# Kernel optimization log

Hardware: AMD Instinct MI355X
Metric: run time of the kernel (lower is better)

## Reference

```python
import jax, jax.numpy as jnp
import numpy as np

WS = 6        # window size -> N = 36 tokens per window
HEADS = 16

def _rel_index(ws):
    coords = np.stack(np.meshgrid(np.arange(ws), np.arange(ws), indexing='ij')).reshape(2, -1)
    rel = coords[:, :, None] - coords[:, None, :] + (ws - 1)
    return jnp.asarray(rel[0] * (2 * ws - 1) + rel[1])  # (N, N) int

REL_IDX = _rel_index(WS)

def _ln(x, g, b, eps=1e-5):
    m = x.mean(-1, keepdims=True)
    v = x.var(-1, keepdims=True)
    return (x - m) / jnp.sqrt(v + eps) * g + b

def setup_inputs() -> dict:
    key = jax.random.key(0)
    ks = jax.random.split(key, 6)
    B, H, W, C = 16, 96, 96, 512
    hid = 4 * C
    s = 0.02
    return {
        'x': jax.random.normal(ks[0], (B, H, W, C), jnp.float32),
        'w_qkv': jax.random.normal(ks[1], (C, 3 * C), jnp.float32) * s,
        'w_proj': jax.random.normal(ks[2], (C, C), jnp.float32) * s,
        'b_proj': jnp.zeros((C,), jnp.float32),
        'rel_bias': jax.random.normal(ks[3], ((2 * WS - 1) ** 2, HEADS), jnp.float32) * s,
        'ln1_g': jnp.ones((C,), jnp.float32), 'ln1_b': jnp.zeros((C,), jnp.float32),
        'ln2_g': jnp.ones((C,), jnp.float32), 'ln2_b': jnp.zeros((C,), jnp.float32),
        'w_fc1': jax.random.normal(ks[4], (C, hid), jnp.float32) * s,
        'b_fc1': jnp.zeros((hid,), jnp.float32),
        'w_fc2': jax.random.normal(ks[5], (hid, C), jnp.float32) * s,
        'b_fc2': jnp.zeros((C,), jnp.float32),
    }

def reference(x, w_qkv, w_proj, b_proj, rel_bias, ln1_g, ln1_b, ln2_g, ln2_b, w_fc1, b_fc1, w_fc2, b_fc2):
    B, H, W, C = x.shape
    h, d, N = HEADS, C // HEADS, WS * WS
    nh, nw = H // WS, W // WS
    # window partition: (B,H,W,C) -> (B*nh*nw, N, C)
    xw = x.reshape(B, nh, WS, nw, WS, C).transpose(0, 1, 3, 2, 4, 5).reshape(B * nh * nw, N, C)
    xn = _ln(xw, ln1_g, ln1_b)
    qkv = xn @ w_qkv
    q, k, v = jnp.split(qkv, 3, axis=-1)
    to_heads = lambda t: t.reshape(-1, N, h, d).transpose(0, 2, 1, 3)  # (B_, h, N, d)
    q = to_heads(q) * (d ** -0.5)
    k = to_heads(k)
    v = to_heads(v)
    attn = jnp.einsum('bhnd,bhmd->bhnm', q, k)
    bias = rel_bias[REL_IDX.reshape(-1)].reshape(N, N, h).transpose(2, 0, 1)  # (h, N, N)
    attn = jax.nn.softmax(attn + bias[None], axis=-1)
    o = jnp.einsum('bhnm,bhmd->bhnd', attn, v).transpose(0, 2, 1, 3).reshape(-1, N, C)
    o = o @ w_proj + b_proj
    # un-window; NOTE: source has no residual around attention (x is replaced)
    x2 = o.reshape(B, nh, nw, WS, WS, C).transpose(0, 1, 3, 2, 4, 5).reshape(B, H, W, C)
    xm = _ln(x2, ln2_g, ln2_b)
    mlp = jax.nn.gelu(xm @ w_fc1 + b_fc1, approximate=False) @ w_fc2 + b_fc2
    return x2 + mlp
```

## Files before the change

### kernel.cpp

```cpp
#include <hip/hip_runtime.h>
#include <stdint.h>

#define TOK 147456
#define CCH 512

typedef __attribute__((ext_vector_type(8))) short short8;
typedef __attribute__((ext_vector_type(4))) float f32x4;

struct alignas(8) US4 { unsigned short a, b, c, d; };

typedef __attribute__((address_space(3))) void lds_void;
typedef const __attribute__((address_space(1))) void gbl_void;

__device__ inline void gload16(const void* g, void* l) {
    __builtin_amdgcn_global_load_lds((gbl_void*)g, (lds_void*)l, 16, 0, 0);
}

__device__ inline unsigned short f2bf(float f) {
    union { float f; unsigned u; } v{f};
    unsigned r = v.u + 0x7fffu + ((v.u >> 16) & 1u);
    return (unsigned short)(r >> 16);
}
__device__ inline float bf2f(unsigned short h) {
    union { unsigned u; float f; } v; v.u = ((unsigned)h) << 16; return v.f;
}

__global__ void wprep(const float* __restrict__ in, unsigned short* __restrict__ out,
                      int K, int N) {
    int idx = blockIdx.x * 256 + threadIdx.x;
    if (idx >= K * N) return;
    int k = idx / N, n = idx % N;
    out[(size_t)n * K + k] = f2bf(in[idx]);
}

__global__ void biasprep(const float* __restrict__ rb, float* __restrict__ bb) {
    int idx = blockIdx.x * 256 + threadIdx.x;
    if (idx >= 16 * 48 * 48) return;
    int h = idx / 2304, rem = idx % 2304, r = rem / 48, c = rem % 48;
    float v = -1e9f;
    if (r < 36 && c < 36) {
        int dy = r / 6 - c / 6 + 5;
        int dx = r % 6 - c % 6 + 5;
        v = rb[(dy * 11 + dx) * 16 + h];
    }
    bb[idx] = v;
}

__global__ __launch_bounds__(256) void ln_k(const float* __restrict__ x,
                                            const float* __restrict__ g,
                                            const float* __restrict__ b,
                                            unsigned short* __restrict__ out, int ntok) {
    int lane = threadIdx.x & 63;
    int tok = blockIdx.x * 4 + (threadIdx.x >> 6);
    if (tok >= ntok) return;
    const float4* xr = (const float4*)(x + (size_t)tok * CCH);
    float4 v0 = xr[lane], v1 = xr[lane + 64];
    float s  = v0.x + v0.y + v0.z + v0.w + v1.x + v1.y + v1.z + v1.w;
    float s2 = v0.x*v0.x + v0.y*v0.y + v0.z*v0.z + v0.w*v0.w
             + v1.x*v1.x + v1.y*v1.y + v1.z*v1.z + v1.w*v1.w;
#pragma unroll
    for (int off = 32; off; off >>= 1) { s += __shfl_xor(s, off); s2 += __shfl_xor(s2, off); }
    float mean = s * (1.f / 512.f);
    float var  = s2 * (1.f / 512.f) - mean * mean;
    float inv  = rsqrtf(var + 1e-5f);
    const float4* gp = (const float4*)g;
    const float4* bp = (const float4*)b;
    float4 g0 = gp[lane], g1 = gp[lane + 64], b0 = bp[lane], b1 = bp[lane + 64];
    US4 o0, o1;
    o0.a = f2bf((v0.x - mean) * inv * g0.x + b0.x);
    o0.b = f2bf((v0.y - mean) * inv * g0.y + b0.y);
    o0.c = f2bf((v0.z - mean) * inv * g0.z + b0.z);
    o0.d = f2bf((v0.w - mean) * inv * g0.w + b0.w);
    o1.a = f2bf((v1.x - mean) * inv * g1.x + b1.x);
    o1.b = f2bf((v1.y - mean) * inv * g1.y + b1.y);
    o1.c = f2bf((v1.z - mean) * inv * g1.z + b1.z);
    o1.d = f2bf((v1.w - mean) * inv * g1.w + b1.w);
    unsigned short* op = out + (size_t)tok * CCH;
    *(US4*)(op + 4 * lane)       = o0;
    *(US4*)(op + 256 + 4 * lane) = o1;
}

__global__ __launch_bounds__(256) void ln_bf(const unsigned short* __restrict__ x,
                                             const float* __restrict__ g,
                                             const float* __restrict__ b,
                                             unsigned short* __restrict__ out, int ntok) {
    int lane = threadIdx.x & 63;
    int tok = blockIdx.x * 4 + (threadIdx.x >> 6);
    if (tok >= ntok) return;
    short8 v = *(const short8*)(x + (size_t)tok * CCH + lane * 8);
    float f[8];
#pragma unroll
    for (int j = 0; j < 8; ++j) f[j] = bf2f((unsigned short)v[j]);
    float s = 0.f, s2 = 0.f;
#pragma unroll
    for (int j = 0; j < 8; ++j) { s += f[j]; s2 += f[j] * f[j]; }
#pragma unroll
    for (int off = 32; off; off >>= 1) { s += __shfl_xor(s, off); s2 += __shfl_xor(s2, off); }
    float mean = s * (1.f / 512.f);
    float var  = s2 * (1.f / 512.f) - mean * mean;
    float inv  = rsqrtf(var + 1e-5f);
    const float4* gp = (const float4*)g + lane * 2;
    const float4* bp = (const float4*)b + lane * 2;
    float4 g0 = gp[0], g1 = gp[1], b0 = bp[0], b1 = bp[1];
    float gg[8] = {g0.x, g0.y, g0.z, g0.w, g1.x, g1.y, g1.z, g1.w};
    float bb[8] = {b0.x, b0.y, b0.z, b0.w, b1.x, b1.y, b1.z, b1.w};
    short8 o;
#pragma unroll
    for (int j = 0; j < 8; ++j) o[j] = (short)f2bf((f[j] - mean) * inv * gg[j] + bb[j]);
    *(short8*)(out + (size_t)tok * CCH + lane * 8) = o;
}

__global__ __launch_bounds__(256) void attn_mfma(const unsigned short* __restrict__ qkv,
                                                 const float* __restrict__ biasb,
                                                 unsigned short* __restrict__ o) {
    __shared__ __align__(16) unsigned short p_lds[4][48 * 64];
    __shared__ __align__(16) unsigned short v_lds[4][32 * 64];

    int tid  = threadIdx.x;
    int wv   = tid >> 6;
    int lane = tid & 63;
    int l15  = lane & 15;
    int g    = lane >> 4;

    int wid = blockIdx.x * 4 + wv;
    int h   = wid & 15;
    int win = wid >> 4;
    int img  = win >> 8;
    int wrow = (win >> 4) & 15;
    int wcol = win & 15;
    int tok_base = (img * 96 + wrow * 6) * 96 + wcol * 6;

    unsigned short* pw = p_lds[wv];
    unsigned short* vw = v_lds[wv];

    #define TOKOF(r) (tok_base + (r) + 90 * ((r) / 6))

    short8 z8 = {};
    for (int e = lane; e < 224; e += 64) {
        if (e < 128) {
            int ch = e >> 2, kst = 32 + (e & 3) * 8;
            *(short8*)(vw + ch * 64 + (kst ^ ((ch & 7) << 3))) = z8;
        } else {
            int ee = e - 128; int q = ee >> 1, kst = 48 + (ee & 1) * 8;
            *(short8*)(pw + q * 64 + (kst ^ ((q & 7) << 3))) = z8;
        }
    }

    for (int e = lane; e < 144; e += 64) {
        int r = e >> 2, c0 = (e & 3) * 8;
        short8 vv = *(const short8*)(qkv + (size_t)TOKOF(r) * 1536 + 1024 + h * 32 + c0);
#pragma unroll
        for (int j = 0; j < 8; ++j) {
            int ch = c0 + j;
            vw[ch * 64 + (r ^ ((ch & 7) << 3))] = (unsigned short)vv[j];
        }
    }

    short8 qf[3], kf[3];
#pragma unroll
    for (int t = 0; t < 3; ++t) {
        int r = t * 16 + l15;
        if (r < 36) {
            size_t ba = (size_t)TOKOF(r) * 1536 + h * 32 + g * 8;
            qf[t] = *(const short8*)(qkv + ba);
            kf[t] = *(const short8*)(qkv + ba + 512);
        } else { qf[t] = z8; kf[t] = z8; }
    }

    f32x4 s[3][3] = {};
#pragma unroll
    for (int mt = 0; mt < 3; ++mt)
#pragma unroll
        for (int nt = 0; nt < 3; ++nt)
            s[mt][nt] = __builtin_amdgcn_mfma_f32_16x16x32_bf16(qf[mt], kf[nt], s[mt][nt], 0, 0, 0);

    const float SCALE = 0.17677669529663687f;
    const float* bh = biasb + h * 2304;
#pragma unroll
    for (int mt = 0; mt < 3; ++mt) {
#pragma unroll
        for (int r = 0; r < 4; ++r) {
            int row = mt * 16 + g * 4 + r;
            const float* bb = bh + row * 48 + l15;
            float v0 = fmaf(s[mt][0][r], SCALE, bb[0]);
            float v1 = fmaf(s[mt][1][r], SCALE, bb[16]);
            float v2 = fmaf(s[mt][2][r], SCALE, bb[32]);
            float m = fmaxf(fmaxf(v0, v1), v2);
#pragma unroll
            for (int off = 1; off < 16; off <<= 1) m = fmaxf(m, __shfl_xor(m, off));
            float e0 = __expf(v0 - m), e1 = __expf(v1 - m), e2 = __expf(v2 - m);
            float sm = e0 + e1 + e2;
#pragma unroll
            for (int off = 1; off < 16; off <<= 1) sm += __shfl_xor(sm, off);
            float inv = 1.f / sm;
            int sw = (row & 7) << 3;
            unsigned short* pr = pw + row * 64;
            pr[(l15)      ^ sw] = f2bf(e0 * inv);
            pr[(16 + l15) ^ sw] = f2bf(e1 * inv);
            pr[(32 + l15) ^ sw] = f2bf(e2 * inv);
        }
    }

    f32x4 oacc[3][2] = {};
#pragma unroll
    for (int ks = 0; ks < 2; ++ks) {
        int kst = ks * 32 + g * 8;
        short8 bfr[2];
#pragma unroll
        for (int nt = 0; nt < 2; ++nt) {
            int c = nt * 16 + l15;
            bfr[nt] = *(const short8*)(vw + c * 64 + (kst ^ ((c & 7) << 3)));
        }
#pragma unroll
        for (int mt = 0; mt < 3; ++mt) {
            int q = mt * 16 + l15;
            short8 pa = *(const short8*)(pw + q * 64 + (kst ^ ((q & 7) << 3)));
#pragma unroll
            for (int nt = 0; nt < 2; ++nt)
                oacc[mt][nt] = __builtin_amdgcn_mfma_f32_16x16x32_bf16(pa, bfr[nt], oacc[mt][nt], 0, 0, 0);
        }
    }

#pragma unroll
    for (int mt = 0; mt < 3; ++mt) {
#pragma unroll
        for (int r = 0; r < 4; ++r) {
            int q = mt * 16 + g * 4 + r;
            if (q < 36) {
                size_t rb = (size_t)TOKOF(q) * 512 + h * 32;
#pragma unroll
                for (int nt = 0; nt < 2; ++nt)
                    o[rb + nt * 16 + l15] = f2bf(oacc[mt][nt][r]);
            }
        }
    }
    #undef TOKOF
}

template <int EPI>
__global__ __launch_bounds__(512, 4) void gemm8(const unsigned short* __restrict__ A,
                                                const unsigned short* __restrict__ Bt,
                                                int M, int N, int K,
                                                const float* __restrict__ bias,
                                                const unsigned short* __restrict__ resid,
                                                void* __restrict__ Cout) {
    extern __shared__ char lds[];
    int tid = threadIdx.x;
    int w = tid >> 6, lane = tid & 63;
    int l15 = lane & 15, grp = lane >> 4;
    int wm = w >> 2, wn = w & 3;

    int nbn = N >> 8;
    int nwg = gridDim.x;
    int q = nwg >> 3, r = nwg & 7;
    int xcd = blockIdx.x & 7, pos_ = blockIdx.x >> 3;
    int wgid = (xcd < r ? xcd * (q + 1) : r * (q + 1) + (xcd - r) * q) + pos_;
    int bm = wgid / nbn, bn = wgid % nbn;

    int NT = K >> 5;

    int u = (tid & 7) ^ ((tid >> 3) & 7);
    int srow = ((tid >> 3) << 1) + (u >> 2);
    int scol = (u & 3) * 8;
    const unsigned short* aSrc = A  + ((size_t)bm * 128 + srow) * (size_t)K + scol;
    const unsigned short* bSrc = Bt + ((size_t)bn * 256 + srow) * (size_t)K + scol;

    #define STAGE(t) do { char* s_ = lds + ((t) % 3) * 24576; size_t ko_ = (size_t)(t) * 32; \
        gload16(aSrc + ko_,                   s_ + tid * 16); \
        gload16(bSrc + ko_,                   s_ + 8192  + tid * 16); \
        gload16(bSrc + ko_ + (size_t)128 * K, s_ + 16384 + tid * 16); } while (0)

    int rpos = (grp + (l15 & 1) * 4) ^ ((l15 >> 1) & 7);
    int aRd = (wm * 32 + (l15 >> 1)) * 128 + rpos * 16;
    int bRd = 8192 + (wn * 32 + (l15 >> 1)) * 128 + rpos * 16;

    f32x4 acc[4][4] = {};

    STAGE(0); STAGE(1);

    for (int t = 0; t < NT; ++t) {
        if (t + 2 < NT) {
            STAGE(t + 2);
            asm volatile("s_waitcnt vmcnt(6)" ::: "memory");
        } else if (t + 1 < NT) {
            asm volatile("s_waitcnt vmcnt(3)" ::: "memory");
        } else {
            asm volatile("s_waitcnt vmcnt(0)" ::: "memory");
        }
        __builtin_amdgcn_s_barrier();
        char* sb = lds + (t % 3) * 24576;
        short8 af[4], bf[4];
#pragma unroll
        for (int m = 0; m < 4; ++m) af[m] = *(const short8*)(sb + aRd + m * 1024);
#pragma unroll
        for (int n = 0; n < 4; ++n) bf[n] = *(const short8*)(sb + bRd + n * 1024);
        asm volatile("s_waitcnt lgkmcnt(0)" ::: "memory");
        __builtin_amdgcn_sched_barrier(0);
        __builtin_amdgcn_s_setprio(1);
#pragma unroll
        for (int m = 0; m < 4; ++m)
#pragma unroll
            for (int n = 0; n < 4; ++n)
                acc[m][n] = __builtin_amdgcn_mfma_f32_16x16x32_bf16(af[m], bf[n], acc[m][n], 0, 0, 0);
        __builtin_amdgcn_s_setprio(0);
        __builtin_amdgcn_s_barrier();
    }
    #undef STAGE

    int row0 = bm * 128 + wm * 64 + grp * 4;
    int col0 = bn * 256 + wn * 64 + l15;
#pragma unroll
    for (int m = 0; m < 4; ++m) {
#pragma unroll
        for (int n = 0; n < 4; ++n) {
            int col = col0 + n * 16;
            float bv = (EPI == 0) ? 0.f : bias[col];
#pragma unroll
            for (int r2 = 0; r2 < 4; ++r2) {
                int row = row0 + m * 16 + r2;
                size_t idx = (size_t)row * N + col;
                float val = acc[m][n][r2] + bv;
                if (EPI == 0) {
                    ((unsigned short*)Cout)[idx] = f2bf(val);
                } else if (EPI == 1) {
                    ((unsigned short*)Cout)[idx] = f2bf(val);
                } else if (EPI == 2) {
                    float u3 = val * val * val;
                    float z2 = 1.5957691216f * (val + 0.044715f * u3);
                    float e = __expf(z2);
                    float th = 1.f - 2.f / (e + 1.f);
                    float ge = 0.5f * val * (1.f + th);
                    ((unsigned short*)Cout)[idx] = f2bf(ge);
                } else {
                    ((float*)Cout)[idx] = val + bf2f(resid[idx]);
                }
            }
        }
    }
}

extern "C" void kernel_launch(void* const* d_in, const int* in_sizes, int n_in,
                              void* d_out, int out_size, void* d_ws, size_t ws_size,
                              hipStream_t stream) {
    const float* x       = (const float*)d_in[0];
    const float* w_qkv   = (const float*)d_in[1];
    const float* w_proj  = (const float*)d_in[2];
    const float* b_proj  = (const float*)d_in[3];
    const float* relb    = (const float*)d_in[4];
    const float* ln1g    = (const float*)d_in[5];
    const float* ln1b    = (const float*)d_in[6];
    const float* ln2g    = (const float*)d_in[7];
    const float* ln2b    = (const float*)d_in[8];
    const float* w_fc1   = (const float*)d_in[9];
    const float* b_fc1   = (const float*)d_in[10];
    const float* w_fc2   = (const float*)d_in[11];
    const float* b_fc2   = (const float*)d_in[12];
    float* out = (float*)d_out;

    hipFuncSetAttribute(reinterpret_cast<const void*>(&gemm8<0>),
                        hipFuncAttributeMaxDynamicSharedMemorySize, 73728);
    hipFuncSetAttribute(reinterpret_cast<const void*>(&gemm8<1>),
                        hipFuncAttributeMaxDynamicSharedMemorySize, 73728);
    hipFuncSetAttribute(reinterpret_cast<const void*>(&gemm8<2>),
                        hipFuncAttributeMaxDynamicSharedMemorySize, 73728);
    hipFuncSetAttribute(reinterpret_cast<const void*>(&gemm8<3>),
                        hipFuncAttributeMaxDynamicSharedMemorySize, 73728);

    char* w = (char*)d_ws;
    unsigned short* wT_qkv  = (unsigned short*)w; w += (size_t)1536 * 512 * 2;
    unsigned short* wT_proj = (unsigned short*)w; w += (size_t)512  * 512 * 2;
    unsigned short* wT_fc1  = (unsigned short*)w; w += (size_t)2048 * 512 * 2;
    unsigned short* wT_fc2  = (unsigned short*)w; w += (size_t)512  * 2048 * 2;
    float* biasb            = (float*)w;          w += (size_t)16 * 48 * 48 * 4;
    size_t wbytes = (size_t)(w - (char*)d_ws);

    int nchunk = 16;
    for (int c = 1; c <= 16; c *= 2) {
        size_t tokc = TOK / c;
        if (wbytes + tokc * 6144 <= ws_size) { nchunk = c; break; }
    }
    size_t tokc = TOK / nchunk;
    unsigned short* buf1 = (unsigned short*)w;
    unsigned short* buf2 = (unsigned short*)(w + tokc * 1024);
    unsigned short* buf3 = (unsigned short*)(w + tokc * 5120);

    wprep<<<(512 * 1536 + 255) / 256, 256, 0, stream>>>(w_qkv,  wT_qkv,  512, 1536);
    wprep<<<(512 * 512  + 255) / 256, 256, 0, stream>>>(w_proj, wT_proj, 512, 512);
    wprep<<<(512 * 2048 + 255) / 256, 256, 0, stream>>>(w_fc1,  wT_fc1,  512, 2048);
    wprep<<<(2048 * 512 + 255) / 256, 256, 0, stream>>>(w_fc2,  wT_fc2,  2048, 512);
    biasprep<<<(16 * 48 * 48 + 255) / 256, 256, 0, stream>>>(relb, biasb);

    int Mc = (int)tokc;
    int gm = Mc / 128;
    int imgs = Mc / 9216;

    for (int c = 0; c < nchunk; ++c) {
        size_t toff = (size_t)c * tokc;
        const float* xc = x + toff * CCH;
        float* outc = out + toff * CCH;

        ln_k<<<Mc / 4, 256, 0, stream>>>(xc, ln1g, ln1b, buf1, Mc);
        gemm8<0><<<gm * 6, 512, 73728, stream>>>(buf1, wT_qkv, Mc, 1536, 512,
                                                 nullptr, nullptr, buf2);
        attn_mfma<<<imgs * 1024, 256, 0, stream>>>(buf2, biasb, buf1);
        gemm8<1><<<gm * 2, 512, 73728, stream>>>(buf1, wT_proj, Mc, 512, 512,
                                                 b_proj, nullptr, buf3);
        ln_bf<<<Mc / 4, 256, 0, stream>>>(buf3, ln2g, ln2b, buf1, Mc);
        gemm8<2><<<gm * 8, 512, 73728, stream>>>(buf1, wT_fc1, Mc, 2048, 512,
                                                 b_fc1, nullptr, buf2);
        gemm8<3><<<gm * 2, 512, 73728, stream>>>(buf2, wT_fc2, Mc, 512, 2048,
                                                 b_fc2, buf3, outc);
    }
}
```

Before: 1.662 ms.

## Load GEMM A operand directly into registers, stage only B through LDS

The GEMM kernel stops staging the A tile through LDS. Each lane now reads its A fragments straight from global memory into registers every K-step, while B keeps a three-slot LDS ring buffer with rotating slot pointers. This removes the second barrier per iteration and shrinks dynamic LDS from 72 KB to 48 KB, aiming to cut LDS traffic and synchronisation. The cost is that A is loaded redundantly by the four waves that share the same rows, and A's global-load latency is not prefetched ahead of the MFMA loop, so it may be exposed on every iteration.

```diff
diff --git a/kernel.cpp b/kernel.cpp
--- a/kernel.cpp
+++ b/kernel.cpp
@@ -262,39 +262,44 @@
     int u = (tid & 7) ^ ((tid >> 3) & 7);
     int srow = ((tid >> 3) << 1) + (u >> 2);
     int scol = (u & 3) * 8;
-    const unsigned short* aSrc = A  + ((size_t)bm * 128 + srow) * (size_t)K + scol;
     const unsigned short* bSrc = Bt + ((size_t)bn * 256 + srow) * (size_t)K + scol;
 
-    #define STAGE(t) do { char* s_ = lds + ((t) % 3) * 24576; size_t ko_ = (size_t)(t) * 32; \
-        gload16(aSrc + ko_,                   s_ + tid * 16); \
-        gload16(bSrc + ko_,                   s_ + 8192  + tid * 16); \
-        gload16(bSrc + ko_ + (size_t)128 * K, s_ + 16384 + tid * 16); } while (0)
+    #define STAGE_B(t, sp) do { size_t ko_ = (size_t)(t) * 32; \
+        gload16(bSrc + ko_,                   (sp) + tid * 16); \
+        gload16(bSrc + ko_ + (size_t)128 * K, (sp) + 8192 + tid * 16); } while (0)
+
+    const unsigned short* aLane = A + ((size_t)bm * 128 + wm * 64 + l15) * (size_t)K + grp * 8;
 
     int rpos = (grp + (l15 & 1) * 4) ^ ((l15 >> 1) & 7);
-    int aRd = (wm * 32 + (l15 >> 1)) * 128 + rpos * 16;
-    int bRd = 8192 + (wn * 32 + (l15 >> 1)) * 128 + rpos * 16;
+    int bRd = (wn * 32 + (l15 >> 1)) * 128 + rpos * 16;
 
     f32x4 acc[4][4] = {};
 
-    STAGE(0); STAGE(1);
+    char* slotA = lds;
+    char* slotB = lds + 16384;
+    char* slotC = lds + 32768;
+    STAGE_B(0, slotA); STAGE_B(1, slotB);
+    char* rd = slotA;
+    char* st = slotC;
 
     for (int t = 0; t < NT; ++t) {
-        if (t + 2 < NT) {
-            STAGE(t + 2);
-            asm volatile("s_waitcnt vmcnt(6)" ::: "memory");
-        } else if (t + 1 < NT) {
-            asm volatile("s_waitcnt vmcnt(3)" ::: "memory");
-        } else {
-            asm volatile("s_waitcnt vmcnt(0)" ::: "memory");
-        }
+        short8 af[4];
+        const unsigned short* ap = aLane + (size_t)t * 32;
+        af[0] = *(const short8*)(ap);
+        af[1] = *(const short8*)(ap + (size_t)16 * K);
+        af[2] = *(const short8*)(ap + (size_t)32 * K);
+        af[3] = *(const short8*)(ap + (size_t)48 * K);
+
+        if (t == 0) asm volatile("s_waitcnt vmcnt(6)" ::: "memory");
         __builtin_amdgcn_s_barrier();
-        char* sb = lds + (t % 3) * 24576;
-        short8 af[4], bf[4];
-#pragma unroll
-        for (int m = 0; m < 4; ++m) af[m] = *(const short8*)(sb + aRd + m * 1024);
-#pragma unroll
-        for (int n = 0; n < 4; ++n) bf[n] = *(const short8*)(sb + bRd + n * 1024);
-        asm volatile("s_waitcnt lgkmcnt(0)" ::: "memory");
+        if (t + 2 < NT) STAGE_B(t + 2, st);
+
+        short8 bf[4];
+#pragma unroll
+        for (int n = 0; n < 4; ++n) bf[n] = *(const short8*)(rd + bRd + n * 1024);
+
+        if (t + 2 < NT) asm volatile("s_waitcnt vmcnt(2) lgkmcnt(0)" ::: "memory");
+        else            asm volatile("s_waitcnt vmcnt(0) lgkmcnt(0)" ::: "memory");
         __builtin_amdgcn_sched_barrier(0);
         __builtin_amdgcn_s_setprio(1);
 #pragma unroll
@@ -303,9 +308,11 @@
             for (int n = 0; n < 4; ++n)
                 acc[m][n] = __builtin_amdgcn_mfma_f32_16x16x32_bf16(af[m], bf[n], acc[m][n], 0, 0, 0);
         __builtin_amdgcn_s_setprio(0);
-        __builtin_amdgcn_s_barrier();
-    }
-    #undef STAGE
+
+        rd = (rd == slotC) ? slotA : rd + 16384;
+        st = (st == slotC) ? slotA : st + 16384;
+    }
+    #undef STAGE_B
 
     int row0 = bm * 128 + wm * 64 + grp * 4;
     int col0 = bn * 256 + wn * 64 + l15;
@@ -358,13 +365,13 @@
     float* out = (float*)d_out;
 
     hipFuncSetAttribute(reinterpret_cast<const void*>(&gemm8<0>),
-                        hipFuncAttributeMaxDynamicSharedMemorySize, 73728);
+                        hipFuncAttributeMaxDynamicSharedMemorySize, 49152);
     hipFuncSetAttribute(reinterpret_cast<const void*>(&gemm8<1>),
-                        hipFuncAttributeMaxDynamicSharedMemorySize, 73728);
+                        hipFuncAttributeMaxDynamicSharedMemorySize, 49152);
     hipFuncSetAttribute(reinterpret_cast<const void*>(&gemm8<2>),
-                        hipFuncAttributeMaxDynamicSharedMemorySize, 73728);
+                        hipFuncAttributeMaxDynamicSharedMemorySize, 49152);
     hipFuncSetAttribute(reinterpret_cast<const void*>(&gemm8<3>),
-                        hipFuncAttributeMaxDynamicSharedMemorySize, 73728);
+                        hipFuncAttributeMaxDynamicSharedMemorySize, 49152);
 
     char* w = (char*)d_ws;
     unsigned short* wT_qkv  = (unsigned short*)w; w += (size_t)1536 * 512 * 2;
@@ -400,15 +407,15 @@
         float* outc = out + toff * CCH;
 
         ln_k<<<Mc / 4, 256, 0, stream>>>(xc, ln1g, ln1b, buf1, Mc);
-        gemm8<0><<<gm * 6, 512, 73728, stream>>>(buf1, wT_qkv, Mc, 1536, 512,
+        gemm8<0><<<gm * 6, 512, 49152, stream>>>(buf1, wT_qkv, Mc, 1536, 512,
                                                  nullptr, nullptr, buf2);
         attn_mfma<<<imgs * 1024, 256, 0, stream>>>(buf2, biasb, buf1);
-        gemm8<1><<<gm * 2, 512, 73728, stream>>>(buf1, wT_proj, Mc, 512, 512,
+        gemm8<1><<<gm * 2, 512, 49152, stream>>>(buf1, wT_proj, Mc, 512, 512,
                                                  b_proj, nullptr, buf3);
         ln_bf<<<Mc / 4, 256, 0, stream>>>(buf3, ln2g, ln2b, buf1, Mc);
-        gemm8<2><<<gm * 8, 512, 73728, stream>>>(buf1, wT_fc1, Mc, 2048, 512,
+        gemm8<2><<<gm * 8, 512, 49152, stream>>>(buf1, wT_fc1, Mc, 2048, 512,
                                                  b_fc1, nullptr, buf2);
-        gemm8<3><<<gm * 2, 512, 73728, stream>>>(buf2, wT_fc2, Mc, 512, 2048,
+        gemm8<3><<<gm * 2, 512, 49152, stream>>>(buf2, wT_fc2, Mc, 512, 2048,
                                                  b_fc2, buf3, outc);
     }
 }
```

New measurement: 2.535 ms. +52.5%, slower.

## Restructure GEMM main loop with register-prefetched B fragments and cheaper GELU epilogue

Applied to the files above, without the earlier changes.

Rewrites the GEMM k-loop as an unrolled-by-two body with rotating LDS stage pointers. The next tile's B fragments are loaded into registers while the current tile's MFMAs run, replacing the per-iteration double barrier with a single wait and barrier. The GELU epilogue is also rewritten algebraically into fewer ops using a hardware reciprocal instead of a division. Risks: the loop now waits with vmcnt(0) every iteration, which exposes global-load latency because only one stage is in flight ahead. The unroll by two assumes NT is even, and the fast reciprocal is slightly less precise.

```diff
diff --git a/kernel.cpp b/kernel.cpp
--- a/kernel.cpp
+++ b/kernel.cpp
@@ -23,6 +23,9 @@
 }
 __device__ inline float bf2f(unsigned short h) {
     union { unsigned u; float f; } v; v.u = ((unsigned)h) << 16; return v.f;
+}
+__device__ inline float frcp(float x) {
+    float r; asm("v_rcp_f32 %0, %1" : "=v"(r) : "v"(x)); return r;
 }
 
 __global__ void wprep(const float* __restrict__ in, unsigned short* __restrict__ out,
@@ -265,46 +268,56 @@
     const unsigned short* aSrc = A  + ((size_t)bm * 128 + srow) * (size_t)K + scol;
     const unsigned short* bSrc = Bt + ((size_t)bn * 256 + srow) * (size_t)K + scol;
 
-    #define STAGE(t) do { char* s_ = lds + ((t) % 3) * 24576; size_t ko_ = (size_t)(t) * 32; \
-        gload16(aSrc + ko_,                   s_ + tid * 16); \
-        gload16(bSrc + ko_,                   s_ + 8192  + tid * 16); \
-        gload16(bSrc + ko_ + (size_t)128 * K, s_ + 16384 + tid * 16); } while (0)
+    #define STAGE(t, sp) do { size_t ko_ = (size_t)(t) * 32; \
+        gload16(aSrc + ko_,                   (sp) + tid * 16); \
+        gload16(bSrc + ko_,                   (sp) + 8192  + tid * 16); \
+        gload16(bSrc + ko_ + (size_t)128 * K, (sp) + 16384 + tid * 16); } while (0)
 
     int rpos = (grp + (l15 & 1) * 4) ^ ((l15 >> 1) & 7);
     int aRd = (wm * 32 + (l15 >> 1)) * 128 + rpos * 16;
     int bRd = 8192 + (wn * 32 + (l15 >> 1)) * 128 + rpos * 16;
 
     f32x4 acc[4][4] = {};
-
-    STAGE(0); STAGE(1);
-
-    for (int t = 0; t < NT; ++t) {
-        if (t + 2 < NT) {
-            STAGE(t + 2);
-            asm volatile("s_waitcnt vmcnt(6)" ::: "memory");
-        } else if (t + 1 < NT) {
-            asm volatile("s_waitcnt vmcnt(3)" ::: "memory");
-        } else {
-            asm volatile("s_waitcnt vmcnt(0)" ::: "memory");
-        }
-        __builtin_amdgcn_s_barrier();
-        char* sb = lds + (t % 3) * 24576;
-        short8 af[4], bf[4];
-#pragma unroll
-        for (int m = 0; m < 4; ++m) af[m] = *(const short8*)(sb + aRd + m * 1024);
-#pragma unroll
-        for (int n = 0; n < 4; ++n) bf[n] = *(const short8*)(sb + bRd + n * 1024);
-        asm volatile("s_waitcnt lgkmcnt(0)" ::: "memory");
-        __builtin_amdgcn_sched_barrier(0);
-        __builtin_amdgcn_s_setprio(1);
-#pragma unroll
-        for (int m = 0; m < 4; ++m)
-#pragma unroll
-            for (int n = 0; n < 4; ++n)
-                acc[m][n] = __builtin_amdgcn_mfma_f32_16x16x32_bf16(af[m], bf[n], acc[m][n], 0, 0, 0);
-        __builtin_amdgcn_s_setprio(0);
-        __builtin_amdgcn_s_barrier();
-    }
+    short8 bP[4], bQ[4];
+
+    char* s0 = lds;
+    char* s1 = lds + 24576;
+    char* s2 = lds + 49152;
+
+    STAGE(0, s0); STAGE(1, s1);
+    asm volatile("s_waitcnt vmcnt(3)" ::: "memory");
+    __builtin_amdgcn_s_barrier();
+#pragma unroll
+    for (int n = 0; n < 4; ++n) bP[n] = *(const short8*)(s0 + bRd + n * 1024);
+
+    char* pc = s0;
+    char* pn = s1;
+    char* ps = s2;
+
+    #define BODY(t, BC, BN) do { \
+        short8 af_[4]; \
+        _Pragma("unroll") \
+        for (int m_ = 0; m_ < 4; ++m_) af_[m_] = *(const short8*)(pc + aRd + m_ * 1024); \
+        _Pragma("unroll") \
+        for (int m_ = 0; m_ < 4; ++m_) \
+            _Pragma("unroll") \
+            for (int n_ = 0; n_ < 4; ++n_) \
+                acc[m_][n_] = __builtin_amdgcn_mfma_f32_16x16x32_bf16(af_[m_], BC[n_], acc[m_][n_], 0, 0, 0); \
+        if ((t) + 1 < NT) { \
+            asm volatile("s_waitcnt vmcnt(0)" ::: "memory");   \
+            __builtin_amdgcn_s_barrier();                       \
+            _Pragma("unroll") \
+            for (int n_ = 0; n_ < 4; ++n_) BN[n_] = *(const short8*)(pn + bRd + n_ * 1024); \
+            if ((t) + 2 < NT) STAGE((t) + 2, ps); \
+        } \
+        { char* t_ = pc; pc = pn; pn = ps; ps = t_; } \
+    } while (0)
+
+    for (int t = 0; t < NT; t += 2) {
+        BODY(t,     bP, bQ);
+        BODY(t + 1, bQ, bP);
+    }
+    #undef BODY
     #undef STAGE
 
     int row0 = bm * 128 + wm * 64 + grp * 4;
@@ -325,11 +338,12 @@
                 } else if (EPI == 1) {
                     ((unsigned short*)Cout)[idx] = f2bf(val);
                 } else if (EPI == 2) {
-                    float u3 = val * val * val;
-                    float z2 = 1.5957691216f * (val + 0.044715f * u3);
-                    float e = __expf(z2);
-                    float th = 1.f - 2.f / (e + 1.f);
-                    float ge = 0.5f * val * (1.f + th);
+                    float t1 = val * val;
+                    float t2 = fmaf(t1, 0.0713548163f, 1.5957691216f);
+                    float z  = val * t2;
+                    float e  = __expf(z);
+                    float rr = frcp(e + 1.f);
+                    float ge = val - val * rr;
                     ((unsigned short*)Cout)[idx] = f2bf(ge);
                 } else {
                     ((float*)Cout)[idx] = val + bf2f(resid[idx]);
```

Measured after the change: 1.651 ms. No clear change (-0.7%).

## Shrink GEMM tiles to 128x128 with 256 threads and double buffering

Applied to the files above, without the earlier changes.

The GEMM moves from a 128x256 tile with 8 waves and triple-buffered LDS (72KB) to a 128x128 tile with 4 waves and double buffering (32KB). Grid sizes double to match. The aim is more resident workgroups per CU and better load balance, at the cost of less reuse per tile and a shallower prefetch. The GELU epilogue is also rewritten to use fewer operations, with a hardware reciprocal replacing the division.

```diff
diff --git a/kernel.cpp b/kernel.cpp
--- a/kernel.cpp
+++ b/kernel.cpp
@@ -23,6 +23,9 @@
 }
 __device__ inline float bf2f(unsigned short h) {
     union { unsigned u; float f; } v; v.u = ((unsigned)h) << 16; return v.f;
+}
+__device__ inline float frcp(float x) {
+    float r; asm("v_rcp_f32 %0, %1" : "=v"(r) : "v"(x)); return r;
 }
 
 __global__ void wprep(const float* __restrict__ in, unsigned short* __restrict__ out,
@@ -238,7 +241,7 @@
 }
 
 template <int EPI>
-__global__ __launch_bounds__(512, 4) void gemm8(const unsigned short* __restrict__ A,
+__global__ __launch_bounds__(256, 4) void gemm8(const unsigned short* __restrict__ A,
                                                 const unsigned short* __restrict__ Bt,
                                                 int M, int N, int K,
                                                 const float* __restrict__ bias,
@@ -248,9 +251,9 @@
     int tid = threadIdx.x;
     int w = tid >> 6, lane = tid & 63;
     int l15 = lane & 15, grp = lane >> 4;
-    int wm = w >> 2, wn = w & 3;
-
-    int nbn = N >> 8;
+    int wm = w >> 1, wn = w & 1;
+
+    int nbn = N >> 7;
     int nwg = gridDim.x;
     int q = nwg >> 3, r = nwg & 7;
     int xcd = blockIdx.x & 7, pos_ = blockIdx.x >> 3;
@@ -263,12 +266,13 @@
     int srow = ((tid >> 3) << 1) + (u >> 2);
     int scol = (u & 3) * 8;
     const unsigned short* aSrc = A  + ((size_t)bm * 128 + srow) * (size_t)K + scol;
-    const unsigned short* bSrc = Bt + ((size_t)bn * 256 + srow) * (size_t)K + scol;
-
-    #define STAGE(t) do { char* s_ = lds + ((t) % 3) * 24576; size_t ko_ = (size_t)(t) * 32; \
-        gload16(aSrc + ko_,                   s_ + tid * 16); \
-        gload16(bSrc + ko_,                   s_ + 8192  + tid * 16); \
-        gload16(bSrc + ko_ + (size_t)128 * K, s_ + 16384 + tid * 16); } while (0)
+    const unsigned short* bSrc = Bt + ((size_t)bn * 128 + srow) * (size_t)K + scol;
+
+    #define STAGE(t, sp) do { size_t ko_ = (size_t)(t) * 32; \
+        gload16(aSrc + ko_,                  (sp) + tid * 16); \
+        gload16(aSrc + ko_ + (size_t)64 * K, (sp) + 4096  + tid * 16); \
+        gload16(bSrc + ko_,                  (sp) + 8192  + tid * 16); \
+        gload16(bSrc + ko_ + (size_t)64 * K, (sp) + 12288 + tid * 16); } while (0)
 
     int rpos = (grp + (l15 & 1) * 4) ^ ((l15 >> 1) & 7);
     int aRd = (wm * 32 + (l15 >> 1)) * 128 + rpos * 16;
@@ -276,24 +280,25 @@
 
     f32x4 acc[4][4] = {};
 
-    STAGE(0); STAGE(1);
+    char* s0 = lds;
+    char* s1 = lds + 16384;
+    STAGE(0, s0);
 
     for (int t = 0; t < NT; ++t) {
-        if (t + 2 < NT) {
-            STAGE(t + 2);
-            asm volatile("s_waitcnt vmcnt(6)" ::: "memory");
-        } else if (t + 1 < NT) {
-            asm volatile("s_waitcnt vmcnt(3)" ::: "memory");
+        char* cur = (t & 1) ? s1 : s0;
+        char* nxt = (t & 1) ? s0 : s1;
+        if (t + 1 < NT) {
+            STAGE(t + 1, nxt);
+            asm volatile("s_waitcnt vmcnt(4)" ::: "memory");
         } else {
             asm volatile("s_waitcnt vmcnt(0)" ::: "memory");
         }
         __builtin_amdgcn_s_barrier();
-        char* sb = lds + (t % 3) * 24576;
         short8 af[4], bf[4];
 #pragma unroll
-        for (int m = 0; m < 4; ++m) af[m] = *(const short8*)(sb + aRd + m * 1024);
-#pragma unroll
-        for (int n = 0; n < 4; ++n) bf[n] = *(const short8*)(sb + bRd + n * 1024);
+        for (int m = 0; m < 4; ++m) af[m] = *(const short8*)(cur + aRd + m * 1024);
+#pragma unroll
+        for (int n = 0; n < 4; ++n) bf[n] = *(const short8*)(cur + bRd + n * 1024);
         asm volatile("s_waitcnt lgkmcnt(0)" ::: "memory");
         __builtin_amdgcn_sched_barrier(0);
         __builtin_amdgcn_s_setprio(1);
@@ -308,7 +313,7 @@
     #undef STAGE
 
     int row0 = bm * 128 + wm * 64 + grp * 4;
-    int col0 = bn * 256 + wn * 64 + l15;
+    int col0 = bn * 128 + wn * 64 + l15;
 #pragma unroll
     for (int m = 0; m < 4; ++m) {
 #pragma unroll
@@ -325,11 +330,12 @@
                 } else if (EPI == 1) {
                     ((unsigned short*)Cout)[idx] = f2bf(val);
                 } else if (EPI == 2) {
-                    float u3 = val * val * val;
-                    float z2 = 1.5957691216f * (val + 0.044715f * u3);
-                    float e = __expf(z2);
-                    float th = 1.f - 2.f / (e + 1.f);
-                    float ge = 0.5f * val * (1.f + th);
+                    float t1 = val * val;
+                    float t2 = fmaf(t1, 0.0713548163f, 1.5957691216f);
+                    float z  = val * t2;
+                    float e  = __expf(z);
+                    float rr = frcp(e + 1.f);
+                    float ge = val - val * rr;
                     ((unsigned short*)Cout)[idx] = f2bf(ge);
                 } else {
                     ((float*)Cout)[idx] = val + bf2f(resid[idx]);
@@ -358,13 +364,13 @@
     float* out = (float*)d_out;
 
     hipFuncSetAttribute(reinterpret_cast<const void*>(&gemm8<0>),
-                        hipFuncAttributeMaxDynamicSharedMemorySize, 73728);
+                        hipFuncAttributeMaxDynamicSharedMemorySize, 32768);
     hipFuncSetAttribute(reinterpret_cast<const void*>(&gemm8<1>),
-                        hipFuncAttributeMaxDynamicSharedMemorySize, 73728);
+                        hipFuncAttributeMaxDynamicSharedMemorySize, 32768);
     hipFuncSetAttribute(reinterpret_cast<const void*>(&gemm8<2>),
-                        hipFuncAttributeMaxDynamicSharedMemorySize, 73728);
+                        hipFuncAttributeMaxDynamicSharedMemorySize, 32768);
     hipFuncSetAttribute(reinterpret_cast<const void*>(&gemm8<3>),
-                        hipFuncAttributeMaxDynamicSharedMemorySize, 73728);
+                        hipFuncAttributeMaxDynamicSharedMemorySize, 32768);
 
     char* w = (char*)d_ws;
     unsigned short* wT_qkv  = (unsigned short*)w; w += (size_t)1536 * 512 * 2;
@@ -400,15 +406,15 @@
         float* outc = out + toff * CCH;
 
         ln_k<<<Mc / 4, 256, 0, stream>>>(xc, ln1g, ln1b, buf1, Mc);
-        gemm8<0><<<gm * 6, 512, 73728, stream>>>(buf1, wT_qkv, Mc, 1536, 512,
-                                                 nullptr, nullptr, buf2);
+        gemm8<0><<<gm * 12, 256, 32768, stream>>>(buf1, wT_qkv, Mc, 1536, 512,
+                                                  nullptr, nullptr, buf2);
         attn_mfma<<<imgs * 1024, 256, 0, stream>>>(buf2, biasb, buf1);
-        gemm8<1><<<gm * 2, 512, 73728, stream>>>(buf1, wT_proj, Mc, 512, 512,
+        gemm8<1><<<gm * 4, 256, 32768, stream>>>(buf1, wT_proj, Mc, 512, 512,
                                                  b_proj, nullptr, buf3);
         ln_bf<<<Mc / 4, 256, 0, stream>>>(buf3, ln2g, ln2b, buf1, Mc);
-        gemm8<2><<<gm * 8, 512, 73728, stream>>>(buf1, wT_fc1, Mc, 2048, 512,
-                                                 b_fc1, nullptr, buf2);
-        gemm8<3><<<gm * 2, 512, 73728, stream>>>(buf2, wT_fc2, Mc, 512, 2048,
+        gemm8<2><<<gm * 16, 256, 32768, stream>>>(buf1, wT_fc1, Mc, 2048, 512,
+                                                  b_fc1, nullptr, buf2);
+        gemm8<3><<<gm * 4, 256, 32768, stream>>>(buf2, wT_fc2, Mc, 512, 2048,
                                                  b_fc2, buf3, outc);
     }
 }
```

After: 1.654 ms. Within noise of the previous version (-0.5%).
